# Performance work log

Hardware: AMD Instinct MI355X
Metric: run time of the kernel (lower is better)

Reference implementation:

```python
import jax, jax.numpy as jnp
import numpy as np

N, F_NODE, DIM, H, K, OUT, L = 200000, 16, 3, 128, 20, 4, 4


def setup_inputs() -> dict:
    key = jax.random.key(0)
    ks = jax.random.split(key, 10)
    x = jax.random.normal(ks[0], (N, F_NODE), jnp.float32)
    pos = jax.random.normal(ks[1], (N, DIM), jnp.float32)
    y = jax.random.normal(ks[2], (DIM,), jnp.float32)
    # eigenvector-like basis, roughly orthonormal columns scale
    phi = jax.random.normal(ks[3], (N, K), jnp.float32) / np.sqrt(N).astype(np.float32)
    # torch Linear convention: W is [out, in], y = x @ W.T + b
    lift_w = jax.random.normal(ks[4], (H, F_NODE + 2 * DIM), jnp.float32) * 0.05
    lift_b = jnp.zeros((H,), jnp.float32)
    lin_w = jax.random.normal(ks[5], (L, H, H), jnp.float32) * 0.05  # per-layer, bias=False
    kernel = jax.random.normal(ks[6], (L, K, H, H), jnp.float32) * 0.05
    lower_w = jax.random.normal(ks[7], (OUT, H), jnp.float32) * 0.05
    lower_b = jnp.zeros((OUT,), jnp.float32)
    return dict(x=x, pos=pos, y=y, phi=phi, lift_w=lift_w, lift_b=lift_b,
                lin_w=lin_w, kernel=kernel, lower_w=lower_w, lower_b=lower_b)


def reference(x, pos, y, phi, lift_w, lift_b, lin_w, kernel, lower_w, lower_b):
    # lift: concat node feats, positions, broadcast global y -> [N, F_NODE+2*DIM]
    h = jnp.concatenate([x, pos, y * jnp.ones_like(pos)], axis=1) @ lift_w.T + lift_b
    # pinv(phi) is identical every layer in the original; compute once. [K, N]
    phi_pinv = jnp.linalg.pinv(phi)
    for l in range(L):
        v = phi_pinv @ h                              # [K, H] spectral coefficients
        rv = jnp.einsum('kij,kj->ki', kernel[l], v)   # batched mode matvec (= nested vmap)
        h = jax.nn.elu(h @ lin_w[l].T + phi @ rv)     # [N, H]
    return h @ lower_w.T + lower_b                    # [N, OUT]
```

## Files before the change

kernel.cpp:

```cpp
#include <hip/hip_runtime.h>
#include <math.h>

#define Nn 200000
#define NT 3125

typedef __attribute__((ext_vector_type(8))) short short8;
typedef __attribute__((ext_vector_type(16))) float floatx16;

#define SWZ4(row, g) (((g) ^ ((row) & 7)) << 2)

__device__ __forceinline__ unsigned rnbf(float x) {
    unsigned u = __builtin_bit_cast(unsigned, x);
    return (u + 0x7fffu + ((u >> 16) & 1u)) >> 16;
}
__device__ __forceinline__ float asf(unsigned u) { return __builtin_bit_cast(float, u); }
__device__ __forceinline__ unsigned packf(float x) {
    unsigned hb = rnbf(x);
    float fh = asf(hb << 16);
    unsigned lb = rnbf(x - fh);
    return hb | (lb << 16);
}
__device__ __forceinline__ void permsplit(const unsigned* e, short8& hi, short8& lo) {
    uint4 h, l;
    h.x = __builtin_amdgcn_perm(e[1], e[0], 0x05040100u);
    h.y = __builtin_amdgcn_perm(e[3], e[2], 0x05040100u);
    h.z = __builtin_amdgcn_perm(e[5], e[4], 0x05040100u);
    h.w = __builtin_amdgcn_perm(e[7], e[6], 0x05040100u);
    l.x = __builtin_amdgcn_perm(e[1], e[0], 0x07060302u);
    l.y = __builtin_amdgcn_perm(e[3], e[2], 0x07060302u);
    l.z = __builtin_amdgcn_perm(e[5], e[4], 0x07060302u);
    l.w = __builtin_amdgcn_perm(e[7], e[6], 0x07060302u);
    hi = __builtin_bit_cast(short8, h);
    lo = __builtin_bit_cast(short8, l);
}
__device__ __forceinline__ void permsplit2(uint4 q0, uint4 q1, short8& hi, short8& lo) {
    unsigned e[8] = { q0.x, q0.y, q0.z, q0.w, q1.x, q1.y, q1.z, q1.w };
    permsplit(e, hi, lo);
}

__device__ __forceinline__ void pt_accum(const unsigned* As, const unsigned* Ph,
                                         float* __restrict__ PTc_blk, int t) {
    int lane = t & 63, w = t >> 6;
    int ln = lane & 31, hw = lane >> 5;
    int j0 = w * 32;
    floatx16 ap;
#pragma unroll
    for (int i = 0; i < 16; i++) ap[i] = 0.f;
#pragma unroll
    for (int ks = 0; ks < 4; ks++) {
        unsigned pa[8], e[8];
#pragma unroll
        for (int j = 0; j < 8; j++) {
            int node = ks * 16 + 8 * hw + j;
            pa[j] = Ph[node * 32 + SWZ4(node, ln >> 2) + (ln & 3)];
            int col = j0 + ln;
            e[j] = As[node * 128 + SWZ4(node, col >> 2) + (col & 3)];
        }
        short8 a_hi, a_lo, b_hi, b_lo;
        permsplit(pa, a_hi, a_lo);
        permsplit(e, b_hi, b_lo);
        ap = __builtin_amdgcn_mfma_f32_32x32x16_bf16(a_hi, b_hi, ap, 0, 0, 0);
        ap = __builtin_amdgcn_mfma_f32_32x32x16_bf16(a_lo, b_hi, ap, 0, 0, 0);
        ap = __builtin_amdgcn_mfma_f32_32x32x16_bf16(a_hi, b_lo, ap, 0, 0, 0);
    }
#pragma unroll
    for (int r = 0; r < 16; r++) {
        int mode = (r & 3) + 8 * (r >> 2) + 4 * hw;
        if (mode < 20) unsafeAtomicAdd(&PTc_blk[mode * 128 + j0 + ln], ap[r]);
    }
}

__device__ __forceinline__ void pt_mfma8(const unsigned* As, const unsigned* Ph,
                                         floatx16& ap, int t) {
    int lane = t & 63, w = t >> 6;
    int ln = lane & 31, hw = lane >> 5;
    int j0 = (w & 3) * 32;
    int nh = w >> 2;
#pragma unroll
    for (int i = 0; i < 16; i++) ap[i] = 0.f;
#pragma unroll
    for (int ks2 = 0; ks2 < 2; ks2++) {
        int ks = nh * 2 + ks2;
        unsigned pa[8], e[8];
#pragma unroll
        for (int j = 0; j < 8; j++) {
            int node = ks * 16 + 8 * hw + j;
            pa[j] = Ph[node * 32 + SWZ4(node, ln >> 2) + (ln & 3)];
            int col = j0 + ln;
            e[j] = As[node * 128 + SWZ4(node, col >> 2) + (col & 3)];
        }
        short8 a_hi, a_lo, b_hi, b_lo;
        permsplit(pa, a_hi, a_lo);
        permsplit(e, b_hi, b_lo);
        ap = __builtin_amdgcn_mfma_f32_32x32x16_bf16(a_hi, b_hi, ap, 0, 0, 0);
        ap = __builtin_amdgcn_mfma_f32_32x32x16_bf16(a_lo, b_hi, ap, 0, 0, 0);
        ap = __builtin_amdgcn_mfma_f32_32x32x16_bf16(a_hi, b_lo, ap, 0, 0, 0);
    }
}

__global__ void ptreduce_k(const float* __restrict__ PTc, float* __restrict__ PT) {
    int j = blockIdx.x * 128 + threadIdx.x;
    float s0 = 0.f, s1 = 0.f, s2 = 0.f, s3 = 0.f;
#pragma unroll
    for (int c = 0; c < 64; c += 4) {
        s0 += PTc[(size_t)c * 2560 + j];
        s1 += PTc[(size_t)(c + 1) * 2560 + j];
        s2 += PTc[(size_t)(c + 2) * 2560 + j];
        s3 += PTc[(size_t)(c + 3) * 2560 + j];
    }
    PT[j] = (s0 + s1) + (s2 + s3);
}

__global__ void bias_fold_k(const float* __restrict__ y, const float* __restrict__ lw,
                            const float* __restrict__ lb, float* __restrict__ b2) {
    int j = threadIdx.x;
    float s = lb[j];
#pragma unroll
    for (int d = 0; d < 3; d++) s += y[d] * lw[j * 22 + 19 + d];
    b2[j] = s;
}

__global__ void wsplit_k(const float* __restrict__ lw, const float* __restrict__ low_w,
                         unsigned short* __restrict__ Wh, unsigned short* __restrict__ Wl,
                         unsigned short* __restrict__ LWh, unsigned short* __restrict__ LWl) {
    int i = blockIdx.x * 256 + threadIdx.x;
    float w;
    unsigned short *ph, *pl;
    int idx;
    if (i < 65536) { w = lw[i]; ph = Wh; pl = Wl; idx = i; }
    else           { w = low_w[i - 65536]; ph = LWh; pl = LWl; idx = i - 65536; }
    unsigned hb = rnbf(w);
    float fh = asf(hb << 16);
    unsigned lb = rnbf(w - fh);
    ph[idx] = (unsigned short)hb;
    pl[idx] = (unsigned short)lb;
}

__global__ __launch_bounds__(256) void lift_k(const float* __restrict__ x,
                                              const float* __restrict__ pos,
                                              const float* __restrict__ phi,
                                              const float* __restrict__ lw,
                                              const float* __restrict__ b2,
                                              unsigned* __restrict__ hpk,
                                              float* __restrict__ PTc) {
    __shared__ union {
        struct { float xs[64][21]; float Wc[20][132]; } a;
        unsigned As[64 * 128];
    } sm;
    __shared__ unsigned Ph[64 * 32];
    int t = threadIdx.x;
    int n0 = blockIdx.x * 64;
    {
        int n = t >> 2, f4 = (t & 3) * 4;
        float4 xv = *(const float4*)(x + (size_t)(n0 + n) * 16 + f4);
        sm.a.xs[n][f4 + 0] = xv.x; sm.a.xs[n][f4 + 1] = xv.y;
        sm.a.xs[n][f4 + 2] = xv.z; sm.a.xs[n][f4 + 3] = xv.w;
    }
    if (t < 192) { int n = t / 3, d = t % 3; sm.a.xs[n][16 + d] = pos[(size_t)(n0 + n) * 3 + d]; }
    if (t < 64) sm.a.xs[t][19] = 1.f;
    for (int idx = t; idx < 2560; idx += 256) {
        int k = idx >> 7, j = idx & 127;
        sm.a.Wc[k][j] = (k < 19) ? lw[j * 22 + k] : b2[j];
    }
    for (int idx = t; idx < 2048; idx += 256) {
        int row = idx >> 5, kk = idx & 31;
        float pv = (kk < 20) ? phi[(size_t)(n0 + row) * 20 + kk] : 0.f;
        Ph[row * 32 + SWZ4(row, kk >> 2) + (kk & 3)] = packf(pv);
    }
    __syncthreads();
    int tx = t & 31, ty = t >> 5, i0 = tx * 4;
    float acc[8][4];
#pragma unroll
    for (int m = 0; m < 8; m++)
#pragma unroll
        for (int c = 0; c < 4; c++) acc[m][c] = 0.f;
#pragma unroll 4
    for (int k = 0; k < 20; k++) {
        float4 w = *(const float4*)&sm.a.Wc[k][i0];
#pragma unroll
        for (int m = 0; m < 8; m++) {
            float a = sm.a.xs[ty + 8 * m][k];
            acc[m][0] += a * w.x; acc[m][1] += a * w.y;
            acc[m][2] += a * w.z; acc[m][3] += a * w.w;
        }
    }
    __syncthreads();
#pragma unroll
    for (int m = 0; m < 8; m++) {
        uint4 o;
        o.x = packf(acc[m][0]); o.y = packf(acc[m][1]);
        o.z = packf(acc[m][2]); o.w = packf(acc[m][3]);
        int row = ty + 8 * m;
        *(uint4*)&hpk[(size_t)(n0 + row) * 128 + i0] = o;
        *(uint4*)&sm.As[row * 128 + SWZ4(row, tx)] = o;
    }
    __syncthreads();
    pt_accum(sm.As, Ph, PTc + (size_t)(blockIdx.x & 63) * 2560, t);
}

__global__ void gram_k(const float* __restrict__ phi, float* __restrict__ G) {
    __shared__ float ph[64 * 20];
    int t = threadIdx.x;
    int i0 = t / 20, j0 = t % 20;
    int p1 = t + 256;
    int i1 = p1 / 20, j1 = p1 % 20;
    float a0 = 0.f, a1 = 0.f;
    for (int tile = blockIdx.x; tile < NT; tile += gridDim.x) {
        const float* src = phi + tile * 1280;
        for (int idx = t; idx < 1280; idx += 256) ph[idx] = src[idx];
        __syncthreads();
        for (int n = 0; n < 64; n++) {
            const float* r = ph + n * 20;
            a0 += r[i0] * r[j0];
            if (p1 < 400) a1 += r[i1] * r[j1];
        }
        __syncthreads();
    }
    unsafeAtomicAdd(&G[t], a0);
    if (p1 < 400) unsafeAtomicAdd(&G[p1], a1);
}

__global__ void ginv_k(const float* __restrict__ G, float* __restrict__ Gi) {
    __shared__ float A[20][40];
    __shared__ float colp[20];
    __shared__ float piv;
    int t = threadIdx.x;
    for (int idx = t; idx < 400; idx += 64) {
        int r = idx / 20, c = idx % 20;
        A[r][c] = G[idx];
        A[r][c + 20] = (r == c) ? 1.f : 0.f;
    }
    __syncthreads();
    for (int p = 0; p < 20; p++) {
        if (t == 0) piv = 1.f / A[p][p];
        __syncthreads();
        for (int c = t; c < 40; c += 64) A[p][c] *= piv;
        __syncthreads();
        if (t < 20) colp[t] = A[t][p];
        __syncthreads();
        for (int e = t; e < 800; e += 64) {
            int r = e / 40, c = e % 40;
            if (r != p) A[r][c] -= colp[r] * A[p][c];
        }
        __syncthreads();
    }
    for (int idx = t; idx < 400; idx += 64) {
        int r = idx / 20, c = idx % 20;
        Gi[idx] = A[r][c + 20];
    }
}

__global__ void rv_k(const float* __restrict__ Gi, const float* __restrict__ PT,
                     const float* __restrict__ kern_l,
                     unsigned short* __restrict__ RVh, unsigned short* __restrict__ RVl) {
    __shared__ __align__(16) float v[128];
    __shared__ float part[128];
    int k = blockIdx.x;
    int t = threadIdx.x;
    if (t < 128) {
        const float* gr = Gi + k * 20;
        float s = 0.f;
#pragma unroll
        for (int m = 0; m < 20; m++) s += gr[m] * PT[m * 128 + t];
        v[t] = s;
    }
    __syncthreads();
    int i = t & 127, half = t >> 7;
    const float* kr = kern_l + (size_t)(k * 128 + i) * 128 + half * 64;
    const float* vk = v + half * 64;
    float acc = 0.f;
#pragma unroll 4
    for (int jj = 0; jj < 64; jj += 4) {
        float4 kv = *(const float4*)(kr + jj);
        float4 vv = *(const float4*)(vk + jj);
        acc += kv.x * vv.x + kv.y * vv.y + kv.z * vv.z + kv.w * vv.w;
    }
    if (half) part[i] = acc;
    __syncthreads();
    if (!half) {
        float rv = acc + part[i];
        unsigned hb = rnbf(rv);
        float fh = asf(hb << 16);
        unsigned lb = rnbf(rv - fh);
        RVh[i * 32 + k] = (unsigned short)hb;
        RVl[i * 32 + k] = (unsigned short)lb;
    }
}

__global__ __launch_bounds__(512, 8) void update_k(unsigned* __restrict__ hpk,
                                                   const float* __restrict__ phi,
                                                   const unsigned short* __restrict__ Wh,
                                                   const unsigned short* __restrict__ Wl,
                                                   const unsigned short* __restrict__ RVh,
                                                   const unsigned short* __restrict__ RVl,
                                                   float* __restrict__ ptn,
                                                   const unsigned short* __restrict__ LWh,
                                                   const unsigned short* __restrict__ LWl,
                                                   const float* __restrict__ low_b,
                                                   float* __restrict__ outp) {
    __shared__ __align__(16) unsigned As[64 * 128];
    __shared__ __align__(16) unsigned Ph[64 * 32];
    int t = threadIdx.x;
    int n0 = blockIdx.x * 64;
    for (int idx = t; idx < 2048; idx += 512) {
        int row = idx >> 5, g = idx & 31;
        uint4 v = *(const uint4*)(hpk + (size_t)(n0 + row) * 128 + g * 4);
        *(uint4*)&As[row * 128 + SWZ4(row, g)] = v;
    }
    for (int idx = t; idx < 2048; idx += 512) {
        int row = idx >> 5, kk = idx & 31;
        float pv = (kk < 20) ? phi[(size_t)(n0 + row) * 20 + kk] : 0.f;
        Ph[row * 32 + SWZ4(row, kk >> 2) + (kk & 3)] = packf(pv);
    }
    __syncthreads();

    int lane = t & 63, w = t >> 6;
    int ln = lane & 31, hw = lane >> 5;
    int r0 = (w >> 2) * 32, ct0 = (w & 3) * 32;
    int arow = r0 + ln;

    floatx16 acc;
#pragma unroll
    for (int i = 0; i < 16; i++) acc[i] = 0.f;

    const unsigned short* whp = Wh + (size_t)(ct0 + ln) * 128 + 8 * hw;
    const unsigned short* wlp = Wl + (size_t)(ct0 + ln) * 128 + 8 * hw;
    const unsigned* abase = As + arow * 128;

#pragma unroll
    for (int ks = 0; ks < 8; ks++) {
        int k0 = ks * 16;
        int ga = 4 * ks + 2 * hw;
        uint4 aq0 = *(const uint4*)(abase + SWZ4(arow, ga));
        uint4 aq1 = *(const uint4*)(abase + SWZ4(arow, ga + 1));
        uint4 wh = *(const uint4*)(whp + k0);
        uint4 wl = *(const uint4*)(wlp + k0);
        short8 a_hi, a_lo;
        permsplit2(aq0, aq1, a_hi, a_lo);
        short8 bh = __builtin_bit_cast(short8, wh);
        short8 bl = __builtin_bit_cast(short8, wl);
        acc = __builtin_amdgcn_mfma_f32_32x32x16_bf16(a_hi, bh, acc, 0, 0, 0);
        acc = __builtin_amdgcn_mfma_f32_32x32x16_bf16(a_lo, bh, acc, 0, 0, 0);
        acc = __builtin_amdgcn_mfma_f32_32x32x16_bf16(a_hi, bl, acc, 0, 0, 0);
    }

    const unsigned* pbase = Ph + arow * 32;
#pragma unroll
    for (int ks = 0; ks < 2; ks++) {
        int k0 = ks * 16;
        int gr = 4 * ks + 2 * hw;
        uint4 q0 = *(const uint4*)(pbase + SWZ4(arow, gr));
        uint4 q1 = *(const uint4*)(pbase + SWZ4(arow, gr + 1));
        short8 a_hi, a_lo;
        permsplit2(q0, q1, a_hi, a_lo);
        short8 bh = __builtin_bit_cast(short8, *(const uint4*)(RVh + (size_t)(ct0 + ln) * 32 + k0 + 8 * hw));
        short8 bl = __builtin_bit_cast(short8, *(const uint4*)(RVl + (size_t)(ct0 + ln) * 32 + k0 + 8 * hw));
        acc = __builtin_amdgcn_mfma_f32_32x32x16_bf16(a_hi, bh, acc, 0, 0, 0);
        acc = __builtin_amdgcn_mfma_f32_32x32x16_bf16(a_lo, bh, acc, 0, 0, 0);
        acc = __builtin_amdgcn_mfma_f32_32x32x16_bf16(a_hi, bl, acc, 0, 0, 0);
    }

    unsigned p0[16];
#pragma unroll
    for (int r = 0; r < 16; r++) {
        float v0 = acc[r];
        v0 = v0 > 0.f ? v0 : __expf(v0) - 1.f;
        p0[r] = packf(v0);
    }
    if (!outp) {
#pragma unroll
        for (int r = 0; r < 16; r++) {
            int row = (r & 3) + 8 * (r >> 2) + 4 * hw;
            hpk[(size_t)(n0 + r0 + row) * 128 + ct0 + ln] = p0[r];
        }
    }
    if (ptn || outp) {
        __syncthreads();
#pragma unroll
        for (int r = 0; r < 16; r++) {
            int row = r0 + (r & 3) + 8 * (r >> 2) + 4 * hw;
            int c0 = ct0 + ln;
            As[row * 128 + SWZ4(row, c0 >> 2) + (c0 & 3)] = p0[r];
        }
        __syncthreads();
        if (outp) {
            float* scr = (float*)Ph;
            int r0o = (w >> 1) * 32, kh = w & 1;
            int arow2 = r0o + ln;
            const unsigned* ab2 = As + arow2 * 128;
            floatx16 ap;
#pragma unroll
            for (int i = 0; i < 16; i++) ap[i] = 0.f;
            if (w < 4) {
#pragma unroll
                for (int kk = 0; kk < 4; kk++) {
                    int ks = kh * 4 + kk;
                    int ga = 4 * ks + 2 * hw;
                    uint4 q0 = *(const uint4*)(ab2 + SWZ4(arow2, ga));
                    uint4 q1 = *(const uint4*)(ab2 + SWZ4(arow2, ga + 1));
                    short8 a_hi, a_lo;
                    permsplit2(q0, q1, a_hi, a_lo);
                    short8 bh = { 0, 0, 0, 0, 0, 0, 0, 0 };
                    short8 bl = { 0, 0, 0, 0, 0, 0, 0, 0 };
                    if (ln < 4) {
                        bh = __builtin_bit_cast(short8, *(const uint4*)(LWh + ln * 128 + ks * 16 + 8 * hw));
                        bl = __builtin_bit_cast(short8, *(const uint4*)(LWl + ln * 128 + ks * 16 + 8 * hw));
                    }
                    ap = __builtin_amdgcn_mfma_f32_32x32x16_bf16(a_hi, bh, ap, 0, 0, 0);
                    ap = __builtin_amdgcn_mfma_f32_32x32x16_bf16(a_lo, bh, ap, 0, 0, 0);
                    ap = __builtin_amdgcn_mfma_f32_32x32x16_bf16(a_hi, bl, ap, 0, 0, 0);
                }
            }
            if (w < 4 && kh == 1 && ln < 4) {
#pragma unroll
                for (int r = 0; r < 16; r++) {
                    int row = (r & 3) + 8 * (r >> 2) + 4 * hw;
                    scr[(w >> 1) * 128 + row * 4 + ln] = ap[r];
                }
            }
            __syncthreads();
            if (w < 4 && kh == 0 && ln < 4) {
                float b = low_b[ln];
#pragma unroll
                for (int r = 0; r < 16; r++) {
                    int row = (r & 3) + 8 * (r >> 2) + 4 * hw;
                    float s = ap[r] + scr[(w >> 1) * 128 + row * 4 + ln] + b;
                    outp[(size_t)(n0 + r0o + row) * 4 + ln] = s;
                }
            }
        } else {
            floatx16 ap;
            pt_mfma8(As, Ph, ap, t);
            int j0 = (w & 3) * 32, nh = w >> 2;
            __syncthreads();
            float* PTs = (float*)As;
            if (nh == 1) {
#pragma unroll
                for (int r = 0; r < 16; r++) {
                    int mode = (r & 3) + 8 * (r >> 2) + 4 * hw;
                    if (mode < 20) PTs[mode * 128 + j0 + ln] = ap[r];
                }
            }
            __syncthreads();
            if (nh == 0) {
                float* blk = ptn + (size_t)(blockIdx.x & 63) * 2560;
#pragma unroll
                for (int r = 0; r < 16; r++) {
                    int mode = (r & 3) + 8 * (r >> 2) + 4 * hw;
                    if (mode < 20) {
                        int idx = mode * 128 + j0 + ln;
                        unsafeAtomicAdd(&blk[idx], ap[r] + PTs[idx]);
                    }
                }
            }
        }
    }
}

extern "C" void kernel_launch(void* const* d_in, const int* in_sizes, int n_in,
                              void* d_out, int out_size, void* d_ws, size_t ws_size,
                              hipStream_t stream) {
    (void)in_sizes; (void)n_in; (void)out_size; (void)ws_size;
    const float* x       = (const float*)d_in[0];
    const float* pos     = (const float*)d_in[1];
    const float* y       = (const float*)d_in[2];
    const float* phi     = (const float*)d_in[3];
    const float* lift_w  = (const float*)d_in[4];
    const float* lift_b  = (const float*)d_in[5];
    const float* lin_w   = (const float*)d_in[6];
    const float* kern    = (const float*)d_in[7];
    const float* lower_w = (const float*)d_in[8];
    const float* lower_b = (const float*)d_in[9];
    float* out = (float*)d_out;

    char* ws = (char*)d_ws;
    unsigned* hpk = (unsigned*)ws;
    size_t off = (size_t)Nn * 128 * 4;
    float* b2  = (float*)(ws + off);       off += 512;
    float* G   = (float*)(ws + off);       off += 1600;
    float* Gi  = (float*)(ws + off);       off += 1600;
    off = (off + 15) & ~(size_t)15;
    float* PT  = (float*)(ws + off);       off += 10240;
    float* PTc = (float*)(ws + off);       off += 64 * 2560 * 4;
    unsigned short* W_hi = (unsigned short*)(ws + off);  off += 131072;
    unsigned short* W_lo = (unsigned short*)(ws + off);  off += 131072;
    unsigned short* RVh  = (unsigned short*)(ws + off);  off += 8192;
    unsigned short* RVl  = (unsigned short*)(ws + off);  off += 8192;
    unsigned short* LWh  = (unsigned short*)(ws + off);  off += 1024;
    unsigned short* LWl  = (unsigned short*)(ws + off);  off += 1024;

    hipMemsetAsync(G, 0, 1600, stream);
    hipMemsetAsync(PTc, 0, 64 * 2560 * 4, stream);
    hipMemsetAsync(RVh, 0, 8192, stream);
    hipMemsetAsync(RVl, 0, 8192, stream);
    bias_fold_k<<<1, 128, 0, stream>>>(y, lift_w, lift_b, b2);
    wsplit_k<<<258, 256, 0, stream>>>(lin_w, lower_w, W_hi, W_lo, LWh, LWl);
    lift_k<<<NT, 256, 0, stream>>>(x, pos, phi, lift_w, b2, hpk, PTc);
    gram_k<<<256, 256, 0, stream>>>(phi, G);
    ginv_k<<<1, 64, 0, stream>>>(G, Gi);
    ptreduce_k<<<20, 128, 0, stream>>>(PTc, PT);

    for (int l = 0; l < 4; l++) {
        rv_k<<<20, 256, 0, stream>>>(Gi, PT, kern + (size_t)l * 20 * 128 * 128, RVh, RVl);
        float* ptc = (l < 3) ? PTc : (float*)nullptr;
        if (ptc) hipMemsetAsync(ptc, 0, 64 * 2560 * 4, stream);
        update_k<<<NT, 512, 0, stream>>>(hpk, phi, W_hi + (size_t)l * 16384,
                                         W_lo + (size_t)l * 16384, RVh, RVl, ptc,
                                         LWh, LWl, lower_b,
                                         (l == 3) ? out : (float*)nullptr);
        if (ptc) ptreduce_k<<<20, 128, 0, stream>>>(PTc, PT);
    }
}
```

Baseline: 616.4 us.

## Fuse partial-sum reduction and buffer zeroing into rv kernel, drop small launches

Folds the lift bias into lift_k, and merges the per-layer PT partial reduction and the zeroing of the next accumulation buffer into the rv kernel. It ping-pongs between two 32-slot partial buffers instead of one 64-slot buffer. This removes several tiny kernel launches and memsets per layer. In exchange, each of the 20 rv blocks redundantly re-reduces all 2560 partial sums, and halving the slots raises atomic contention in update_k.

```diff
diff --git a/kernel.cpp b/kernel.cpp
--- a/kernel.cpp
+++ b/kernel.cpp
@@ -98,26 +98,62 @@
     }
 }
 
-__global__ void ptreduce_k(const float* __restrict__ PTc, float* __restrict__ PT) {
-    int j = blockIdx.x * 128 + threadIdx.x;
-    float s0 = 0.f, s1 = 0.f, s2 = 0.f, s3 = 0.f;
-#pragma unroll
-    for (int c = 0; c < 64; c += 4) {
-        s0 += PTc[(size_t)c * 2560 + j];
-        s1 += PTc[(size_t)(c + 1) * 2560 + j];
-        s2 += PTc[(size_t)(c + 2) * 2560 + j];
-        s3 += PTc[(size_t)(c + 3) * 2560 + j];
-    }
-    PT[j] = (s0 + s1) + (s2 + s3);
-}
-
-__global__ void bias_fold_k(const float* __restrict__ y, const float* __restrict__ lw,
-                            const float* __restrict__ lb, float* __restrict__ b2) {
-    int j = threadIdx.x;
-    float s = lb[j];
-#pragma unroll
-    for (int d = 0; d < 3; d++) s += y[d] * lw[j * 22 + 19 + d];
-    b2[j] = s;
+__global__ void rvfused_k(const float* __restrict__ Gi,
+                          const float* __restrict__ ptRead,
+                          float* __restrict__ ptZero,
+                          const float* __restrict__ kern_l,
+                          unsigned short* __restrict__ RVh,
+                          unsigned short* __restrict__ RVl) {
+    __shared__ __align__(16) float PTs[2560];
+    __shared__ __align__(16) float v[128];
+    __shared__ float part[128];
+    int k = blockIdx.x;
+    int t = threadIdx.x;
+    for (int idx = t; idx < 2560; idx += 256) {
+        float s0 = 0.f, s1 = 0.f, s2 = 0.f, s3 = 0.f;
+#pragma unroll
+        for (int c = 0; c < 32; c += 4) {
+            s0 += ptRead[(size_t)c * 2560 + idx];
+            s1 += ptRead[(size_t)(c + 1) * 2560 + idx];
+            s2 += ptRead[(size_t)(c + 2) * 2560 + idx];
+            s3 += ptRead[(size_t)(c + 3) * 2560 + idx];
+        }
+        PTs[idx] = (s0 + s1) + (s2 + s3);
+    }
+    {
+        float4 z = { 0.f, 0.f, 0.f, 0.f };
+        for (int idx = t; idx < 1024; idx += 256)
+            *(float4*)&ptZero[((size_t)k * 1024 + idx) * 4] = z;
+    }
+    __syncthreads();
+    if (t < 128) {
+        const float* gr = Gi + k * 20;
+        float s = 0.f;
+#pragma unroll
+        for (int m = 0; m < 20; m++) s += gr[m] * PTs[m * 128 + t];
+        v[t] = s;
+    }
+    __syncthreads();
+    int i = t & 127, half = t >> 7;
+    const float* kr = kern_l + (size_t)(k * 128 + i) * 128 + half * 64;
+    const float* vk = v + half * 64;
+    float acc = 0.f;
+#pragma unroll 4
+    for (int jj = 0; jj < 64; jj += 4) {
+        float4 kv = *(const float4*)(kr + jj);
+        float4 vv = *(const float4*)(vk + jj);
+        acc += kv.x * vv.x + kv.y * vv.y + kv.z * vv.z + kv.w * vv.w;
+    }
+    if (half) part[i] = acc;
+    __syncthreads();
+    if (!half) {
+        float rv = acc + part[i];
+        unsigned hb = rnbf(rv);
+        float fh = asf(hb << 16);
+        unsigned lb = rnbf(rv - fh);
+        RVh[i * 32 + k] = (unsigned short)hb;
+        RVl[i * 32 + k] = (unsigned short)lb;
+    }
 }
 
 __global__ void wsplit_k(const float* __restrict__ lw, const float* __restrict__ low_w,
@@ -140,7 +176,8 @@
                                               const float* __restrict__ pos,
                                               const float* __restrict__ phi,
                                               const float* __restrict__ lw,
-                                              const float* __restrict__ b2,
+                                              const float* __restrict__ lb,
+                                              const float* __restrict__ yg,
                                               unsigned* __restrict__ hpk,
                                               float* __restrict__ PTc) {
     __shared__ union {
@@ -160,7 +197,14 @@
     if (t < 64) sm.a.xs[t][19] = 1.f;
     for (int idx = t; idx < 2560; idx += 256) {
         int k = idx >> 7, j = idx & 127;
-        sm.a.Wc[k][j] = (k < 19) ? lw[j * 22 + k] : b2[j];
+        float wv;
+        if (k < 19) {
+            wv = lw[j * 22 + k];
+        } else {
+            wv = lb[j] + yg[0] * lw[j * 22 + 19] + yg[1] * lw[j * 22 + 20]
+                       + yg[2] * lw[j * 22 + 21];
+        }
+        sm.a.Wc[k][j] = wv;
     }
     for (int idx = t; idx < 2048; idx += 256) {
         int row = idx >> 5, kk = idx & 31;
@@ -195,7 +239,7 @@
         *(uint4*)&sm.As[row * 128 + SWZ4(row, tx)] = o;
     }
     __syncthreads();
-    pt_accum(sm.As, Ph, PTc + (size_t)(blockIdx.x & 63) * 2560, t);
+    pt_accum(sm.As, Ph, PTc + (size_t)(blockIdx.x & 31) * 2560, t);
 }
 
 __global__ void gram_k(const float* __restrict__ phi, float* __restrict__ G) {
@@ -247,43 +291,6 @@
     for (int idx = t; idx < 400; idx += 64) {
         int r = idx / 20, c = idx % 20;
         Gi[idx] = A[r][c + 20];
-    }
-}
-
-__global__ void rv_k(const float* __restrict__ Gi, const float* __restrict__ PT,
-                     const float* __restrict__ kern_l,
-                     unsigned short* __restrict__ RVh, unsigned short* __restrict__ RVl) {
-    __shared__ __align__(16) float v[128];
-    __shared__ float part[128];
-    int k = blockIdx.x;
-    int t = threadIdx.x;
-    if (t < 128) {
-        const float* gr = Gi + k * 20;
-        float s = 0.f;
-#pragma unroll
-        for (int m = 0; m < 20; m++) s += gr[m] * PT[m * 128 + t];
-        v[t] = s;
-    }
-    __syncthreads();
-    int i = t & 127, half = t >> 7;
-    const float* kr = kern_l + (size_t)(k * 128 + i) * 128 + half * 64;
-    const float* vk = v + half * 64;
-    float acc = 0.f;
-#pragma unroll 4
-    for (int jj = 0; jj < 64; jj += 4) {
-        float4 kv = *(const float4*)(kr + jj);
-        float4 vv = *(const float4*)(vk + jj);
-        acc += kv.x * vv.x + kv.y * vv.y + kv.z * vv.z + kv.w * vv.w;
-    }
-    if (half) part[i] = acc;
-    __syncthreads();
-    if (!half) {
-        float rv = acc + part[i];
-        unsigned hb = rnbf(rv);
-        float fh = asf(hb << 16);
-        unsigned lb = rnbf(rv - fh);
-        RVh[i * 32 + k] = (unsigned short)hb;
-        RVl[i * 32 + k] = (unsigned short)lb;
     }
 }
 
@@ -443,7 +450,7 @@
             }
             __syncthreads();
             if (nh == 0) {
-                float* blk = ptn + (size_t)(blockIdx.x & 63) * 2560;
+                float* blk = ptn + (size_t)(blockIdx.x & 31) * 2560;
 #pragma unroll
                 for (int r = 0; r < 16; r++) {
                     int mode = (r & 3) + 8 * (r >> 2) + 4 * hw;
@@ -488,26 +495,24 @@
     unsigned short* RVl  = (unsigned short*)(ws + off);  off += 8192;
     unsigned short* LWh  = (unsigned short*)(ws + off);  off += 1024;
     unsigned short* LWl  = (unsigned short*)(ws + off);  off += 1024;
+    (void)b2; (void)PT;
+    float* ptbuf[2] = { PTc, PTc + 32 * 2560 };
 
     hipMemsetAsync(G, 0, 1600, stream);
     hipMemsetAsync(PTc, 0, 64 * 2560 * 4, stream);
-    hipMemsetAsync(RVh, 0, 8192, stream);
-    hipMemsetAsync(RVl, 0, 8192, stream);
-    bias_fold_k<<<1, 128, 0, stream>>>(y, lift_w, lift_b, b2);
+    hipMemsetAsync(RVh, 0, 16384, stream);
     wsplit_k<<<258, 256, 0, stream>>>(lin_w, lower_w, W_hi, W_lo, LWh, LWl);
-    lift_k<<<NT, 256, 0, stream>>>(x, pos, phi, lift_w, b2, hpk, PTc);
+    lift_k<<<NT, 256, 0, stream>>>(x, pos, phi, lift_w, lift_b, y, hpk, ptbuf[0]);
     gram_k<<<256, 256, 0, stream>>>(phi, G);
     ginv_k<<<1, 64, 0, stream>>>(G, Gi);
-    ptreduce_k<<<20, 128, 0, stream>>>(PTc, PT);
 
     for (int l = 0; l < 4; l++) {
-        rv_k<<<20, 256, 0, stream>>>(Gi, PT, kern + (size_t)l * 20 * 128 * 128, RVh, RVl);
-        float* ptc = (l < 3) ? PTc : (float*)nullptr;
-        if (ptc) hipMemsetAsync(ptc, 0, 64 * 2560 * 4, stream);
+        rvfused_k<<<20, 256, 0, stream>>>(Gi, ptbuf[l & 1], ptbuf[(l + 1) & 1],
+                                          kern + (size_t)l * 20 * 128 * 128, RVh, RVl);
+        float* ptc = (l < 3) ? ptbuf[(l + 1) & 1] : (float*)nullptr;
         update_k<<<NT, 512, 0, stream>>>(hpk, phi, W_hi + (size_t)l * 16384,
                                          W_lo + (size_t)l * 16384, RVh, RVl, ptc,
                                          LWh, LWl, lower_b,
                                          (l == 3) ? out : (float*)nullptr);
-        if (ptc) ptreduce_k<<<20, 128, 0, stream>>>(PTc, PT);
-    }
-}
+    }
+}
```

After: 689.4 us. 11.8% more time.
